# Kernel tuning notes

Hardware: AMD Instinct MI355X
Metric: run time of the kernel (lower is better)

Reference implementation:

```python
import jax, jax.numpy as jnp
import numpy as np

B, P, D = 64, 196, 2048      # batch, num_pixels, encoder_dim
E, H, A = 512, 512, 512      # embed, hidden, attention dims
V, S = 32000, 22             # vocab, caption seq_len


def setup_inputs() -> dict:
    key = jax.random.key(0)
    ks = jax.random.split(key, 24)
    sc = 0.02
    features = jax.random.normal(ks[0], (B, P, D), jnp.float32)
    captions = jax.random.randint(ks[1], (S, B), 0, V)
    caption_lengths = jax.random.randint(ks[2], (B,), 3, S + 1)
    caption_lengths = caption_lengths.at[0].set(S)  # make max static = S
    p = lambda i, shp: sc * jax.random.normal(ks[i], shp, jnp.float32)
    return {
        "features": features,
        "captions": captions,
        "caption_lengths": caption_lengths,
        "emb_W": p(3, (V, E)),
        "We": p(4, (D, A)), "be": p(5, (A,)),
        "Wd": p(6, (H, A)), "bd": p(7, (A,)),
        "wf": p(8, (A, 1)), "bf": p(9, (1,)),
        "Wih": p(10, (4 * H, E + D)), "Whh": p(11, (4 * H, H)),
        "bih": p(12, (4 * H,)), "bhh": p(13, (4 * H,)),
        "Wh0": p(14, (D, H)), "bh0": p(15, (H,)),
        "Wc0": p(16, (D, H)), "bc0": p(17, (H,)),
        "Wbeta": p(18, (H, D)), "bbeta": p(19, (D,)),
        "Wout": p(20, (H, V)), "bout": p(21, (V,)),
    }


def reference(features, captions, caption_lengths, emb_W, We, be, Wd, bd, wf, bf,
              Wih, Whh, bih, bhh, Wh0, bh0, Wc0, bc0, Wbeta, bbeta, Wout, bout):
    # sort batch by caption length, descending
    sort_ind = jnp.argsort(-caption_lengths)
    lens = caption_lengths[sort_ind]
    enc = features[sort_ind]                     # [B,P,D]
    caps = captions.T[sort_ind]                  # [B,S]
    emb = emb_W[caps]                            # [B,S,E]
    mean_enc = enc.mean(axis=1)
    h0 = mean_enc @ Wh0 + bh0
    c0 = mean_enc @ Wc0 + bc0
    decode_lengths = lens - 1
    T = captions.shape[0] - 2                    # max(decode_lengths) - 1, static
    att1 = enc @ We + be                         # [B,P,A], step-invariant
    emb_t = jnp.moveaxis(emb[:, :T, :], 1, 0)    # [T,B,E]
    t_idx = jnp.arange(T)

    def step(carry, inp):
        h, c = carry
        e_t, t = inp
        att2 = h @ Wd + bd                                   # [B,A]
        scores = (jax.nn.relu(att1 + att2[:, None, :]) @ wf)[..., 0] + bf[0]  # [B,P]
        alpha = jax.nn.softmax(scores, axis=1)
        awe = jnp.einsum('bpd,bp->bd', enc, alpha)           # [B,D]
        gate = jax.nn.sigmoid(h @ Wbeta + bbeta)             # [B,D]
        x = jnp.concatenate([e_t, gate * awe], axis=1)       # [B,E+D]
        g = x @ Wih.T + bih + h @ Whh.T + bhh                # [B,4H]
        i, f, gg, o = jnp.split(g, 4, axis=1)                # torch LSTMCell gate order
        c_new = jax.nn.sigmoid(f) * c + jax.nn.sigmoid(i) * jnp.tanh(gg)
        h_new = jax.nn.sigmoid(o) * jnp.tanh(c_new)
        preds = h_new @ Wout + bout                          # [B,V] (dropout in eval = identity)
        m = (decode_lengths > t)[:, None].astype(preds.dtype)
        return (h_new, c_new), (preds * m, alpha * m)

    (_, _), (preds, alphas) = jax.lax.scan(step, (h0, c0), (emb_t, t_idx))
    predictions = jnp.moveaxis(preds, 0, 1)   # [B,T,V]
    alphas = jnp.moveaxis(alphas, 0, 1)       # [B,T,P]
    return predictions, caps, lens, alphas, sort_ind
```

## Files before the change

### kernel.cpp

```cpp
#include <hip/hip_runtime.h>
#include <stdint.h>

typedef short s16x8 __attribute__((ext_vector_type(8)));
typedef short s16x4 __attribute__((ext_vector_type(4)));
typedef float f32x4 __attribute__((ext_vector_type(4)));
typedef unsigned short u16;
typedef unsigned int u32;

#define DEV __device__ __forceinline__

DEV float bf2f(u16 v){ union{float f; unsigned u;} x; x.u = ((unsigned)v)<<16; return x.f; }
DEV u16 f2bf(float f){ union{float f; unsigned u;} x; x.f = f; unsigned r = x.u + 0x7fffu + ((x.u>>16)&1u); return (u16)(r>>16); }
DEV float sigm(float x){ return 1.f/(1.f + __expf(-x)); }

DEV u32  aL(const u32* p){ return __hip_atomic_load(p, __ATOMIC_RELAXED, __HIP_MEMORY_SCOPE_AGENT); }
DEV void aS(u32* p, u32 v){ __hip_atomic_store(p, v, __ATOMIC_RELAXED, __HIP_MEMORY_SCOPE_AGENT); }
DEV float aLf(const float* p){ return __hip_atomic_load(p, __ATOMIC_RELAXED, __HIP_MEMORY_SCOPE_AGENT); }
DEV void aSf(float* p, float v){ __hip_atomic_store(p, v, __ATOMIC_RELAXED, __HIP_MEMORY_SCOPE_AGENT); }


enum { EPI_F32=0, EPI_BF16=1, EPI_H0C0=2, EPI_PREDS=3 };

struct EpiParams {
  float* out0; long ldo;
  u16* outb;
  const float* bias0;
  const int* declen;
  float* c; u16* xh;
};

template<int BM, int BN, int EPI, bool SWAPXY, int SWZM>
__global__ __launch_bounds__(256) void gemm_bt(
    const u16* __restrict__ A, long lda,
    const u16* __restrict__ B, long ldb,
    int K, EpiParams ep)
{
  constexpr int MF = BM/64;
  constexpr int NF = BN/16;
  constexpr int CHA = BM*8, CH = CHA + BN*8;
  constexpr int NST = CH/256;
  __shared__ char smem[(BM+BN)*128];
  const int tid = threadIdx.x;
  const int w = tid>>6, lane = tid&63;

  long arow0, brow0;
  if constexpr (SWZM > 0) {
    int id = blockIdx.x, tot = gridDim.x;
    int q = tot>>3, r = tot&7, xcd = id&7, idx = id>>3;
    int cid = (xcd<r) ? xcd*(q+1)+idx : r*(q+1)+(xcd-r)*q+idx;
    arow0 = (long)(cid % SWZM)*BM; brow0 = (long)(cid / SWZM)*BN;
  } else if constexpr (SWAPXY) { arow0 = (long)blockIdx.x*BM; brow0 = (long)blockIdx.y*BN; }
  else { arow0 = (long)blockIdx.y*BM; brow0 = (long)blockIdx.x*BN; }

  const u16* gsrc[NST]; int ldst[NST];
  #pragma unroll
  for (int i=0;i<NST;++i){
    int c = i*256 + tid;
    if (i*256 < CHA){
      int row = c>>3, k16 = c&7;
      gsrc[i] = A + (arow0+row)*lda + k16*8;
      ldst[i] = row*128 + ((k16*16) ^ ((row&7)<<4));
    } else {
      int cb = c - CHA; int row = cb>>3, k16 = cb&7;
      gsrc[i] = B + (brow0+row)*ldb + k16*8;
      ldst[i] = BM*128 + row*128 + ((k16*16) ^ ((row&7)<<4));
    }
  }

  f32x4 acc[MF][NF];
  #pragma unroll
  for (int i=0;i<MF;++i)
    #pragma unroll
    for (int j=0;j<NF;++j) acc[i][j] = (f32x4){0.f,0.f,0.f,0.f};

  const int KT = K >> 6;
  s16x8 st[NST];
  #pragma unroll
  for (int i=0;i<NST;++i) st[i] = *(const s16x8*)(gsrc[i]);

  char* Al = smem;
  for (int kk=0; kk<KT; ++kk){
    #pragma unroll
    for (int i=0;i<NST;++i) *(s16x8*)(smem + ldst[i]) = st[i];
    __syncthreads();
    if (kk+1 < KT){
      long kb = (long)(kk+1)*64;
      #pragma unroll
      for (int i=0;i<NST;++i) st[i] = *(const s16x8*)(gsrc[i] + kb);
    }
    #pragma unroll
    for (int ks = 0; ks < 2; ++ks) {
      s16x8 af[MF], bfr[NF];
      const int kboff = ks*64 + ((lane>>4)<<4);
      #pragma unroll
      for (int mf=0; mf<MF; ++mf) {
        int r = w*(16*MF) + mf*16 + (lane&15);
        af[mf] = *(const s16x8*)(Al + r*128 + (kboff ^ ((r&7)<<4)));
      }
      #pragma unroll
      for (int nf=0; nf<NF; ++nf) {
        int r = nf*16 + (lane&15);
        bfr[nf] = *(const s16x8*)(Al + BM*128 + r*128 + (kboff ^ ((r&7)<<4)));
      }
      #pragma unroll
      for (int mf=0; mf<MF; ++mf)
        #pragma unroll
        for (int nf=0; nf<NF; ++nf)
          acc[mf][nf] = __builtin_amdgcn_mfma_f32_16x16x32_bf16(bfr[nf], af[mf], acc[mf][nf], 0,0,0);
    }
    __syncthreads();
  }

  #pragma unroll
  for (int mf=0; mf<MF; ++mf)
    #pragma unroll
    for (int nf=0; nf<NF; ++nf){
      long m = arow0 + w*(16*MF) + mf*16 + (lane&15);
      long n0 = brow0 + nf*16 + ((lane>>4)<<2);
      f32x4 bv = *(const f32x4*)&ep.bias0[n0];
      f32x4 v = acc[mf][nf] + bv;
      if constexpr (EPI == EPI_F32) {
        *(f32x4*)&ep.out0[m*ep.ldo + n0] = v;
      } else if constexpr (EPI == EPI_BF16) {
        u16 o[4];
        #pragma unroll
        for (int r=0;r<4;++r) o[r] = f2bf(v[r]);
        *(s16x4*)&ep.outb[m*ep.ldo + n0] = *(s16x4*)o;
      } else if constexpr (EPI == EPI_H0C0) {
        if (n0 < 512){
          u16 o[4];
          #pragma unroll
          for (int r=0;r<4;++r) o[r] = f2bf(v[r]);
          *(s16x4*)&ep.xh[m*2560 + 2048 + n0] = *(s16x4*)o;
        } else {
          *(f32x4*)&ep.c[m*512 + (n0-512)] = v;
        }
      } else {
        int tt = (int)(m>>6), b = (int)(m&63);
        if (ep.declen[b] > tt)
          *(f32x4*)&ep.out0[(long)b*640000 + (long)tt*32000 + n0] = v;
      }
    }
}

DEV void gsync(u32* flags, u32* epochw, u32 ep, int blk, int tid){
  __syncthreads();
  if (blk == 0){
    if (tid == 0) aS(flags, ep);
    if (tid < 256){
      while (aL(flags + tid*16) < ep) __builtin_amdgcn_s_sleep(4);
    }
    __syncthreads();
    if (tid == 0) aS(epochw, ep);
  } else {
    if (tid == 0){
      aS(flags + blk*16, ep);
      while (aL(epochw) < ep) __builtin_amdgcn_s_sleep(8);
    }
    __syncthreads();
  }
}

struct FusedArgs {
  const u16* att1; const u16* enc;
  const u16* wmisc; const u16* wcat2;
  const float* gst; const float* wf; const float* bfp;
  const int* declen; const float* bmisc; const int* nact;
  u16* xh20; float* y0p;
  float* part; int* cnt; float* c; u16* hall;
  float* alph; u32* bar;
};

__global__ __launch_bounds__(512) void steps_fused(FusedArgs fa)
{
  __shared__ char smem[61440];
  __shared__ float wred[8];
  __shared__ int lastf;
  const int blk = blockIdx.x, tid = threadIdx.x;
  const int w = tid>>6, lane = tid&63;
  const int mstrip = w>>1, nhalf = w&1;
  u32* flags = fa.bar;
  u32* epochw = fa.bar + 4096;
  u32 ep = 0;

  for (int t=0; t<20; ++t){
    u16* cur = fa.xh20 + (long)t*163840;
    u16* nxt = cur + 163840;
    u32* cur32 = (u32*)cur;
    u32* nxt32 = (u32*)nxt;

    if (blk < 80){
      const int brow0 = blk*32;
      f32x4 acc = {0,0,0,0};
      #pragma unroll
      for (int r=0; r<2; ++r){
        u32 sa[16];
        #pragma unroll
        for (int i=0;i<16;++i){
          int c = i*512 + tid;
          int row = c>>7, kp = c&127;
          sa[i] = *(const u32*)(cur32 + (long)row*1280 + 1024 + r*128 + kp);
        }
        s16x8 sb[2];
        #pragma unroll
        for (int i=0;i<2;++i){
          int c = i*512 + tid;
          int row = c>>5, k16 = c&31;
          sb[i] = *(const s16x8*)(fa.wmisc + (long)(brow0+row)*512 + r*256 + k16*8);
        }
        #pragma unroll
        for (int i=0;i<16;++i){
          int c = i*512 + tid;
          int row = c>>7, kp = c&127;
          *(u32*)(smem + row*512 + ((kp*4) ^ ((row&7)<<4))) = sa[i];
        }
        #pragma unroll
        for (int i=0;i<2;++i){
          int c = i*512 + tid;
          int row = c>>5, k16 = c&31;
          *(s16x8*)(smem + 32768 + row*512 + ((k16*16) ^ ((row&7)<<4))) = sb[i];
        }
        __syncthreads();
        #pragma unroll
        for (int ks=0; ks<8; ++ks){
          int kboff = ks*64 + ((lane>>4)<<4);
          int ra = mstrip*16 + (lane&15);
          s16x8 af = *(const s16x8*)(smem + ra*512 + (kboff ^ ((ra&7)<<4)));
          int rb = nhalf*16 + (lane&15);
          s16x8 bf = *(const s16x8*)(smem + 32768 + rb*512 + (kboff ^ ((rb&7)<<4)));
          acc = __builtin_amdgcn_mfma_f32_16x16x32_bf16(bf, af, acc, 0,0,0);
        }
        __syncthreads();
      }
      int m = mstrip*16 + (lane&15);
      int n0 = brow0 + nhalf*16 + ((lane>>4)<<2);
      #pragma unroll
      for (int j=0;j<4;++j)
        aSf(fa.y0p + (long)m*2560 + n0 + j, acc[j] + fa.bmisc[n0+j]);
    }
    gsync(flags, epochw, ++ep, blk, tid);

    {
      const int b = blk & 63, s = blk >> 6;
      const int na = fa.nact[t];
      if (b >= na){
        if (s == 0){
          for (int i=tid; i<196; i+=512)
            fa.alph[((long)b*20 + t)*196 + i] = 0.f;
        }
      } else {
      float* att2p = (float*)smem;
      float* wfp   = att2p + 576;
      float* alps  = wfp + 576;
      float* awe_p = alps + 208;
      {
        int kg0 = tid>>6, j = tid&63;
        att2p[kg0*72 + j] = aLf(fa.y0p + (long)b*2560 + 2048 + tid);
        wfp[kg0*72 + j]   = fa.wf[tid];
      }
      __syncthreads();
      const float bfv = fa.bfp[0];
      const int pg = lane>>3, kg = lane&7;
      #pragma unroll
      for (int pass=0; pass<4; ++pass){
        int p = pass*64 + w*8 + pg;
        if (p < 196){
          const u16* ap = fa.att1 + (((long)(b*196 + p))<<9) + kg*64;
          float sa = 0.f;
          #pragma unroll
          for (int i=0;i<8;++i){
            s16x8 v = *(const s16x8*)(ap + i*8);
            #pragma unroll
            for (int q=0;q<8;++q){
              float x = bf2f((u16)v[q]) + att2p[kg*72 + i*8 + q];
              x = fmaxf(x, 0.f);
              sa += x * wfp[kg*72 + i*8 + q];
            }
          }
          sa += __shfl_xor(sa, 1);
          sa += __shfl_xor(sa, 2);
          sa += __shfl_xor(sa, 4);
          if (kg == 0) alps[p] = sa + bfv;
        }
      }
      __syncthreads();
      float v = (tid < 196) ? alps[tid] : -3.4e38f;
      float m8 = v;
      #pragma unroll
      for (int off=32; off; off>>=1) m8 = fmaxf(m8, __shfl_xor(m8, off));
      if (lane == 0) wred[w] = m8;
      __syncthreads();
      float mx = wred[0];
      #pragma unroll
      for (int i=1;i<8;++i) mx = fmaxf(mx, wred[i]);
      float e = (tid < 196) ? __expf(v - mx) : 0.f;
      float s8 = e;
      #pragma unroll
      for (int off=32; off; off>>=1) s8 += __shfl_xor(s8, off);
      __syncthreads();
      if (lane == 0) wred[w] = s8;
      __syncthreads();
      float den = wred[0]+wred[1]+wred[2]+wred[3]+wred[4]+wred[5]+wred[6]+wred[7];
      float inv = 1.f/den;
      if (tid < 196){
        float a = e*inv;
        alps[tid] = a;
        if (s==0) fa.alph[((long)b*20 + t)*196 + tid] = (fa.declen[b] > t) ? a : 0.f;
      }
      __syncthreads();
      const int d0 = s*512 + lane*8;
      const u16* ebase = fa.enc + (((long)b*196)<<11) + d0;
      float a8[8] = {0,0,0,0,0,0,0,0};
      int p = w;
      for (; p+24 < 196; p += 32){
        s16x8 e0 = __builtin_nontemporal_load((const s16x8*)(ebase + ((long)p<<11)));
        s16x8 e1 = __builtin_nontemporal_load((const s16x8*)(ebase + ((long)(p+8)<<11)));
        s16x8 e2 = __builtin_nontemporal_load((const s16x8*)(ebase + ((long)(p+16)<<11)));
        s16x8 e3 = __builtin_nontemporal_load((const s16x8*)(ebase + ((long)(p+24)<<11)));
        float a0 = alps[p], a1 = alps[p+8], a2 = alps[p+16], a3 = alps[p+24];
        #pragma unroll
        for (int q=0;q<8;++q) a8[q] += a0*bf2f((u16)e0[q]);
        #pragma unroll
        for (int q=0;q<8;++q) a8[q] += a1*bf2f((u16)e1[q]);
        #pragma unroll
        for (int q=0;q<8;++q) a8[q] += a2*bf2f((u16)e2[q]);
        #pragma unroll
        for (int q=0;q<8;++q) a8[q] += a3*bf2f((u16)e3[q]);
      }
      for (; p < 196; p += 8){
        s16x8 ev = __builtin_nontemporal_load((const s16x8*)(ebase + ((long)p<<11)));
        float a = alps[p];
        #pragma unroll
        for (int q=0;q<8;++q) a8[q] += a*bf2f((u16)ev[q]);
      }
      *(f32x4*)&awe_p[w*512 + lane*8]     = (f32x4){a8[0],a8[1],a8[2],a8[3]};
      *(f32x4*)&awe_p[w*512 + lane*8 + 4] = (f32x4){a8[4],a8[5],a8[6],a8[7]};
      __syncthreads();
      if (tid < 256){
        int c0 = 2*tid;
        float s0 = 0.f, s1 = 0.f;
        #pragma unroll
        for (int g=0; g<8; ++g){ s0 += awe_p[g*512 + c0]; s1 += awe_p[g*512 + c0 + 1]; }
        float g0 = sigm(aLf(fa.y0p + (long)b*2560 + s*512 + c0));
        float g1 = sigm(aLf(fa.y0p + (long)b*2560 + s*512 + c0 + 1));
        u32 pk = (u32)f2bf(g0*s0) | ((u32)f2bf(g1*s1) << 16);
        aS(cur32 + (long)b*1280 + s*256 + tid, pk);
      }
      __syncthreads();
      }
    }
    gsync(flags, epochw, ++ep, blk, tid);

    {
      const int ntile = blk & 63, split = blk >> 6;
      f32x4 acc = {0,0,0,0};
      #pragma unroll
      for (int r=0; r<2; ++r){
        const int kbw = split*640 + r*320;
        const int kbd = split*320 + r*160;
        u32 sa[20];
        #pragma unroll
        for (int i=0;i<20;++i){
          int c = i*512 + tid;
          int row = c/160, kp = c%160;
          sa[i] = *(const u32*)(cur32 + (long)row*1280 + kbd + kp);
        }
        s16x8 sb[3];
        #pragma unroll
        for (int i=0;i<3;++i){
          int c = i*512 + tid;
          if (c < 1280){
            int row = c/40, k16 = c%40;
            sb[i] = *(const s16x8*)(fa.wcat2 + (long)(ntile*32+row)*2560 + kbw + k16*8);
          }
        }
        #pragma unroll
        for (int i=0;i<20;++i){
          int c = i*512 + tid;
          int row = c/160, kp = c%160;
          *(u32*)(smem + row*640 + ((kp*4) ^ ((row&7)<<4))) = sa[i];
        }
        #pragma unroll
        for (int i=0;i<3;++i){
          int c = i*512 + tid;
          if (c < 1280){
            int row = c/40, k16 = c%40;
            *(s16x8*)(smem + 40960 + row*640 + ((k16*16) ^ ((row&7)<<4))) = sb[i];
          }
        }
        __syncthreads();
        #pragma unroll
        for (int ks=0; ks<10; ++ks){
          int kboff = ks*64 + ((lane>>4)<<4);
          int ra = mstrip*16 + (lane&15);
          s16x8 af = *(const s16x8*)(smem + ra*640 + (kboff ^ ((ra&7)<<4)));
          int rb = nhalf*16 + (lane&15);
          s16x8 bf = *(const s16x8*)(smem + 40960 + rb*640 + (kboff ^ ((rb&7)<<4)));
          acc = __builtin_amdgcn_mfma_f32_16x16x32_bf16(bf, af, acc, 0,0,0);
        }
        __syncthreads();
      }
      {
        float* PS = fa.part + (long)split*(64*2048);
        int m = mstrip*16 + (lane&15);
        int n0 = ntile*32 + nhalf*16 + ((lane>>4)<<2);
        #pragma unroll
        for (int j=0;j<4;++j) aSf(PS + (long)m*2048 + n0 + j, acc[j]);
      }
      __syncthreads();
      if (tid==0){
        int v = __hip_atomic_fetch_add(fa.cnt + t*64 + ntile, 1,
                                       __ATOMIC_RELAXED, __HIP_MEMORY_SCOPE_AGENT);
        lastf = (v == 3);
      }
      __syncthreads();
      if (lastf && tid < 256){
        int b = tid>>2, jp = tid&3;
        u16 h2[2];
        #pragma unroll
        for (int jj=0; jj<2; ++jj){
          int jl = jp*2 + jj;
          int j = ntile*8 + jl;
          float g4[4];
          #pragma unroll
          for (int gi=0; gi<4; ++gi){
            long n = (long)ntile*32 + jl*4 + gi;
            float sg = fa.gst[((long)t*64 + b)*2048 + n];
            #pragma unroll
            for (int sp=0; sp<4; ++sp)
              sg += aLf(fa.part + (long)sp*(64*2048) + (long)b*2048 + n);
            g4[gi] = sg;
          }
          float cc = aLf(fa.c + b*512 + j);
          float cn = sigm(g4[1])*cc + sigm(g4[0])*tanhf(g4[2]);
          float hn = sigm(g4[3])*tanhf(cn);
          aSf(fa.c + b*512 + j, cn);
          h2[jj] = f2bf(hn);
        }
        u32 pk = (u32)h2[0] | ((u32)h2[1] << 16);
        aS(nxt32 + (long)b*1280 + 1024 + ntile*4 + jp, pk);
        *(u32*)&fa.hall[((long)t*64 + b)*512 + ntile*8 + jp*2] = pk;
      }
    }
    if (t < 19) gsync(flags, epochw, ++ep, blk, tid);
  }
}

__global__ __launch_bounds__(256) void transpose_bf16(
    const float* __restrict__ in, u16* __restrict__ out, int R, int C)
{
  __shared__ float t[64][65];
  const int bx = blockIdx.x*64, by = blockIdx.y*64;
  const int tx = threadIdx.x & 63, ty = threadIdx.x >> 6;
  #pragma unroll
  for (int i=0;i<16;++i){ int r = i*4+ty; t[r][tx] = in[(long)(by+r)*C + bx+tx]; }
  __syncthreads();
  #pragma unroll
  for (int i=0;i<16;++i){ int cc = i*4+ty; out[(long)(bx+cc)*R + by+tx] = f2bf(t[tx][cc]); }
}

__global__ void sort_k(const int* __restrict__ cl, const int* __restrict__ captions,
                       int* __restrict__ sidx, int* __restrict__ declen,
                       float* __restrict__ outCaps, float* __restrict__ outLens,
                       float* __restrict__ outSidx, int* __restrict__ cnt,
                       u32* __restrict__ bar, int* __restrict__ nact)
{
  __shared__ int s_idx[64];
  __shared__ int s_dl[64];
  int i = threadIdx.x;
  int li = cl[i];
  int rank = 0;
  for (int j=0;j<64;++j){ int lj = cl[j]; rank += (lj>li) || (lj==li && j<i); }
  s_idx[rank] = i;
  __syncthreads();
  int src = s_idx[i];
  sidx[i] = src;
  int L = cl[src];
  declen[i] = L - 1;
  s_dl[i] = L - 1;
  outLens[i] = (float)L;
  outSidx[i] = (float)src;
  for (int s=0;s<22;++s) outCaps[i*22+s] = (float)captions[s*64 + src];
  for (int s=0;s<20;++s) cnt[s*64 + i] = 0;
  for (int s=i; s<4160; s+=64) bar[s] = 0u;
  __syncthreads();
  if (i < 20){
    int c = 0;
    for (int j=0;j<64;++j) c += (s_dl[j] > i);
    nact[i] = c;
  }
}

__global__ __launch_bounds__(256) void prep_enc(
    const float* __restrict__ features, const int* __restrict__ sidx,
    u16* __restrict__ enc, u16* __restrict__ meanb)
{
  __shared__ float red[4][256];
  int b = blockIdx.x >> 3, oct = blockIdx.x & 7;
  int lv = threadIdx.x & 63, g = threadIdx.x >> 6;
  int d0 = oct*256 + lv*4;
  const float* src = features + (long)sidx[b]*(196*2048) + d0;
  float acc[4] = {0.f,0.f,0.f,0.f};
  for (int p=g; p<196; p+=4){
    f32x4 v = *(const f32x4*)(src + (long)p*2048);
    u16 o[4];
    #pragma unroll
    for (int q=0;q<4;++q){ acc[q] += v[q]; o[q] = f2bf(v[q]); }
    *(s16x4*)(enc + ((long)b*196 + p)*2048 + d0) = *(s16x4*)o;
  }
  #pragma unroll
  for (int q=0;q<4;++q) red[g][lv*4+q] = acc[q];
  __syncthreads();
  if (threadIdx.x < 64){
    u16 mo[4];
    #pragma unroll
    for (int q=0;q<4;++q){
      float s = red[0][threadIdx.x*4+q] + red[1][threadIdx.x*4+q]
              + red[2][threadIdx.x*4+q] + red[3][threadIdx.x*4+q];
      mo[q] = f2bf(s*(1.f/196.f));
    }
    *(s16x4*)(meanb + b*2048 + oct*256 + threadIdx.x*4) = *(s16x4*)mo;
  }
}

__global__ void emb_gather(const int* __restrict__ captions, const int* __restrict__ sidx,
                           const float* __restrict__ embW, u16* __restrict__ out)
{
  int idx = blockIdx.x*256 + threadIdx.x;
  int row = idx >> 6; int e0 = (idx & 63)*8;
  int t = row >> 6, b = row & 63;
  int tok = captions[t*64 + sidx[b]];
  const float* s = embW + (long)tok*512 + e0;
  f32x4 v0 = *(const f32x4*)s, v1 = *(const f32x4*)(s+4);
  u16 o[8];
  #pragma unroll
  for (int q=0;q<4;++q){ o[q] = f2bf(v0[q]); o[4+q] = f2bf(v1[q]); }
  *(s16x8*)(out + (long)row*512 + e0) = *(s16x8*)o;
}

__global__ void build_wcat2(const float* __restrict__ Wih, const float* __restrict__ Whh,
                            u16* __restrict__ out)
{
  long idx = (long)blockIdx.x*256 + threadIdx.x;
  int r = (int)(idx / 320);
  int kc = (int)(idx % 320) * 8;
  int j = r>>2, g = r&3;
  int orow = g*512 + j;
  const float* s = (kc < 2048) ? (Wih + (long)orow*2560 + 512 + kc)
                               : (Whh + (long)orow*512 + (kc - 2048));
  f32x4 v0 = *(const f32x4*)s, v1 = *(const f32x4*)(s+4);
  u16 o[8];
  #pragma unroll
  for (int q=0;q<4;++q){ o[q] = f2bf(v0[q]); o[4+q] = f2bf(v1[q]); }
  *(s16x8*)(out + (long)r*2560 + kc) = *(s16x8*)o;
}

__global__ void build_wihe(const float* __restrict__ Wih, u16* __restrict__ out)
{
  int idx = blockIdx.x*256 + threadIdx.x;
  int r = idx >> 6; int kc = (idx & 63)*8;
  int j = r>>2, g = r&3;
  const float* s = Wih + (long)(g*512+j)*2560 + kc;
  f32x4 v0 = *(const f32x4*)s, v1 = *(const f32x4*)(s+4);
  u16 o[8];
  #pragma unroll
  for (int q=0;q<4;++q){ o[q] = f2bf(v0[q]); o[4+q] = f2bf(v1[q]); }
  *(s16x8*)(out + (long)r*512 + kc) = *(s16x8*)o;
}

__global__ void build_bias(const float* bih, const float* bhh, const float* bbeta,
                           const float* bd, const float* bh0, const float* bc0,
                           float* bstat, float* bmisc, float* bhc)
{
  int idx = blockIdx.x*256 + threadIdx.x;
  if (idx < 2048){ int j = idx>>2, g = idx&3; bstat[idx] = bih[g*512+j] + bhh[g*512+j]; }
  else if (idx < 4608){ int k = idx-2048; bmisc[k] = (k<2048) ? bbeta[k] : bd[k-2048]; }
  else if (idx < 5632){ int k = idx-4608; bhc[k] = (k<512) ? bh0[k] : bc0[k-512]; }
}

static constexpr long OFF_ENC   = 0;
static constexpr long OFF_ATT1  = 51380224;
static constexpr long OFF_WOUTT = 64225280;
static constexpr long OFF_WET   = 96993280;
static constexpr long OFF_WMISC = 99090432;
static constexpr long OFF_WHC   = 101711872;
static constexpr long OFF_WCAT2 = 105906176;
static constexpr long OFF_WIHE  = 116391936;
static constexpr long OFF_EMBB  = 118489088;
static constexpr long OFF_GST   = 119799808;
static constexpr long OFF_HALL  = 130285568;
static constexpr long OFF_MEANB = 131596288;
static constexpr long OFF_C     = 132513792;
static constexpr long OFF_Y0P   = 132644864;
static constexpr long OFF_BSTAT = 133955584;
static constexpr long OFF_BMISC = 133963776;
static constexpr long OFF_BHC   = 133974016;
static constexpr long OFF_SIDX  = 133978112;
static constexpr long OFF_DECL  = 133978368;
static constexpr long OFF_CNT   = 133978624;
static constexpr long OFF_BAR   = 133983744;
static constexpr long OFF_NACT  = 134000384;
static constexpr long OFF_XH20  = 134017024;
static constexpr long OFF_PART  = OFF_WHC;

extern "C" void kernel_launch(void* const* d_in, const int* in_sizes, int n_in,
                              void* d_out, int out_size, void* d_ws, size_t ws_size,
                              hipStream_t stream)
{
  (void)in_sizes; (void)n_in; (void)out_size; (void)ws_size;
  const float* features = (const float*)d_in[0];
  const int*   captions = (const int*)d_in[1];
  const int*   caplen   = (const int*)d_in[2];
  const float* embW     = (const float*)d_in[3];
  const float* We       = (const float*)d_in[4];
  const float* be       = (const float*)d_in[5];
  const float* Wd       = (const float*)d_in[6];
  const float* bd       = (const float*)d_in[7];
  const float* wf       = (const float*)d_in[8];
  const float* bfp      = (const float*)d_in[9];
  const float* Wih      = (const float*)d_in[10];
  const float* Whh      = (const float*)d_in[11];
  const float* bih      = (const float*)d_in[12];
  const float* bhh      = (const float*)d_in[13];
  const float* Wh0      = (const float*)d_in[14];
  const float* bh0      = (const float*)d_in[15];
  const float* Wc0      = (const float*)d_in[16];
  const float* bc0      = (const float*)d_in[17];
  const float* Wbeta    = (const float*)d_in[18];
  const float* bbeta    = (const float*)d_in[19];
  const float* Wout     = (const float*)d_in[20];
  const float* bout     = (const float*)d_in[21];

  char* ws = (char*)d_ws;
  u16*   enc   = (u16*)(ws + OFF_ENC);
  u16*   att1  = (u16*)(ws + OFF_ATT1);
  u16*   woutt = (u16*)(ws + OFF_WOUTT);
  u16*   wet   = (u16*)(ws + OFF_WET);
  u16*   wmisc = (u16*)(ws + OFF_WMISC);
  u16*   whc   = (u16*)(ws + OFF_WHC);
  u16*   wcat2 = (u16*)(ws + OFF_WCAT2);
  u16*   wihe  = (u16*)(ws + OFF_WIHE);
  u16*   embb  = (u16*)(ws + OFF_EMBB);
  float* gst   = (float*)(ws + OFF_GST);
  u16*   hall  = (u16*)(ws + OFF_HALL);
  u16*   meanb = (u16*)(ws + OFF_MEANB);
  float* cbuf  = (float*)(ws + OFF_C);
  float* y0p   = (float*)(ws + OFF_Y0P);
  float* bstat = (float*)(ws + OFF_BSTAT);
  float* bmisc = (float*)(ws + OFF_BMISC);
  float* bhc   = (float*)(ws + OFF_BHC);
  int*   sidx  = (int*)(ws + OFF_SIDX);
  int*   declen= (int*)(ws + OFF_DECL);
  int*   cnt   = (int*)(ws + OFF_CNT);
  u32*   bar   = (u32*)(ws + OFF_BAR);
  int*   nact  = (int*)(ws + OFF_NACT);
  u16*   xh20  = (u16*)(ws + OFF_XH20);
  float* part  = (float*)(ws + OFF_PART);

  float* outP    = (float*)d_out;
  float* outCaps = outP + 40960000;
  float* outLens = outCaps + 1408;
  float* outAlph = outLens + 64;
  float* outSidx = outAlph + 250880;

  sort_k<<<1,64,0,stream>>>(caplen, captions, sidx, declen, outCaps, outLens, outSidx, cnt, bar, nact);
  prep_enc<<<512,256,0,stream>>>(features, sidx, enc, meanb);
  emb_gather<<<320,256,0,stream>>>(captions, sidx, embW, embb);
  transpose_bf16<<<dim3(8,32),256,0,stream>>>(We,    wet,              2048, 512);
  transpose_bf16<<<dim3(32,8),256,0,stream>>>(Wbeta, wmisc,            512, 2048);
  transpose_bf16<<<dim3(8,8), 256,0,stream>>>(Wd,    wmisc + 2048*512, 512, 512);
  transpose_bf16<<<dim3(8,32),256,0,stream>>>(Wh0,   whc,              2048, 512);
  transpose_bf16<<<dim3(8,32),256,0,stream>>>(Wc0,   whc + 512*2048,   2048, 512);
  transpose_bf16<<<dim3(500,8),256,0,stream>>>(Wout, woutt,            512, 32000);
  build_wcat2<<<2560,256,0,stream>>>(Wih, Whh, wcat2);
  build_wihe<<<512,256,0,stream>>>(Wih, wihe);
  build_bias<<<22,256,0,stream>>>(bih,bhh,bbeta,bd,bh0,bc0,bstat,bmisc,bhc);

  { EpiParams ep{}; ep.bias0 = bhc; ep.xh = xh20; ep.c = cbuf;
    gemm_bt<64,64,EPI_H0C0,false,0><<<dim3(16,1),256,0,stream>>>(meanb, 2048, whc, 2048, 2048, ep); }
  { EpiParams ep{}; ep.outb = att1; ep.ldo = 512; ep.bias0 = be;
    gemm_bt<128,128,EPI_BF16,true,0><<<dim3(98,4),256,0,stream>>>(enc, 2048, wet, 2048, 2048, ep); }
  { EpiParams ep{}; ep.out0 = gst; ep.ldo = 2048; ep.bias0 = bstat;
    gemm_bt<128,64,EPI_F32,false,0><<<dim3(32,10),256,0,stream>>>(embb, 512, wihe, 512, 512, ep); }

  {
    FusedArgs fa;
    fa.att1 = att1; fa.enc = enc; fa.wmisc = wmisc; fa.wcat2 = wcat2;
    fa.gst = gst; fa.wf = wf; fa.bfp = bfp; fa.declen = declen; fa.bmisc = bmisc;
    fa.nact = nact;
    fa.xh20 = xh20; fa.y0p = y0p;
    fa.part = part; fa.cnt = cnt; fa.c = cbuf; fa.hall = hall;
    fa.alph = outAlph; fa.bar = bar;
    void* kargs[1] = { &fa };
    hipLaunchCooperativeKernel((const void*)steps_fused, dim3(256), dim3(512),
                               kargs, 0, stream);
  }

  { EpiParams ep{}; ep.out0 = outP; ep.bias0 = bout; ep.declen = declen;
    gemm_bt<128,128,EPI_PREDS,false,10><<<2500,256,0,stream>>>(hall, 512, woutt, 512, 512, ep); }
}
```

Measured before the change: 1.320 ms.

## Fold att2 and gate projections into attention phase, removing a grid barrier per step

Drops the per-step MFMA phase in which 80 blocks computed h@[Wbeta|Wd] into a global buffer, and the grid-wide sync that followed it. Each attention block now computes its own att2 vector and its 512-wide gate slice with a scalar dot product over h, reading a new k-pair-interleaved bf16 weight layout. The partial-sum and cell-state buffers are transposed to a column-major [n][batch] layout for coalesced access, and the alpha masking by decode length is dropped. The cost is redundant weight reads: every block re-reads the Wd column set, and the four blocks of each batch row share the Wbeta slices.

```diff
diff --git a/kernel.cpp b/kernel.cpp
--- a/kernel.cpp
+++ b/kernel.cpp
@@ -133,7 +133,8 @@
           for (int r=0;r<4;++r) o[r] = f2bf(v[r]);
           *(s16x4*)&ep.xh[m*2560 + 2048 + n0] = *(s16x4*)o;
         } else {
-          *(f32x4*)&ep.c[m*512 + (n0-512)] = v;
+          #pragma unroll
+          for (int r=0;r<4;++r) ep.c[(long)(n0-512+r)*64 + m] = v[r];
         }
       } else {
         int tt = (int)(m>>6), b = (int)(m&63);
@@ -163,10 +164,10 @@
 
 struct FusedArgs {
   const u16* att1; const u16* enc;
-  const u16* wmisc; const u16* wcat2;
+  const u32* wmt; const u16* wcat2;
   const float* gst; const float* wf; const float* bfp;
   const int* declen; const float* bmisc; const int* nact;
-  u16* xh20; float* y0p;
+  u16* xh20;
   float* part; int* cnt; float* c; u16* hall;
   float* alph; u32* bar;
 };
@@ -189,57 +190,6 @@
     u32* cur32 = (u32*)cur;
     u32* nxt32 = (u32*)nxt;
 
-    if (blk < 80){
-      const int brow0 = blk*32;
-      f32x4 acc = {0,0,0,0};
-      #pragma unroll
-      for (int r=0; r<2; ++r){
-        u32 sa[16];
-        #pragma unroll
-        for (int i=0;i<16;++i){
-          int c = i*512 + tid;
-          int row = c>>7, kp = c&127;
-          sa[i] = *(const u32*)(cur32 + (long)row*1280 + 1024 + r*128 + kp);
-        }
-        s16x8 sb[2];
-        #pragma unroll
-        for (int i=0;i<2;++i){
-          int c = i*512 + tid;
-          int row = c>>5, k16 = c&31;
-          sb[i] = *(const s16x8*)(fa.wmisc + (long)(brow0+row)*512 + r*256 + k16*8);
-        }
-        #pragma unroll
-        for (int i=0;i<16;++i){
-          int c = i*512 + tid;
-          int row = c>>7, kp = c&127;
-          *(u32*)(smem + row*512 + ((kp*4) ^ ((row&7)<<4))) = sa[i];
-        }
-        #pragma unroll
-        for (int i=0;i<2;++i){
-          int c = i*512 + tid;
-          int row = c>>5, k16 = c&31;
-          *(s16x8*)(smem + 32768 + row*512 + ((k16*16) ^ ((row&7)<<4))) = sb[i];
-        }
-        __syncthreads();
-        #pragma unroll
-        for (int ks=0; ks<8; ++ks){
-          int kboff = ks*64 + ((lane>>4)<<4);
-          int ra = mstrip*16 + (lane&15);
-          s16x8 af = *(const s16x8*)(smem + ra*512 + (kboff ^ ((ra&7)<<4)));
-          int rb = nhalf*16 + (lane&15);
-          s16x8 bf = *(const s16x8*)(smem + 32768 + rb*512 + (kboff ^ ((rb&7)<<4)));
-          acc = __builtin_amdgcn_mfma_f32_16x16x32_bf16(bf, af, acc, 0,0,0);
-        }
-        __syncthreads();
-      }
-      int m = mstrip*16 + (lane&15);
-      int n0 = brow0 + nhalf*16 + ((lane>>4)<<2);
-      #pragma unroll
-      for (int j=0;j<4;++j)
-        aSf(fa.y0p + (long)m*2560 + n0 + j, acc[j] + fa.bmisc[n0+j]);
-    }
-    gsync(flags, epochw, ++ep, blk, tid);
-
     {
       const int b = blk & 63, s = blk >> 6;
       const int na = fa.nact[t];
@@ -253,17 +203,36 @@
       float* wfp   = att2p + 576;
       float* alps  = wfp + 576;
       float* awe_p = alps + 208;
+      float* hs    = awe_p + 4096;
+      float* garr  = hs + 512;
+      if (tid < 256){
+        u32 hp = *(const u32*)(cur32 + (long)b*1280 + 1024 + tid);
+        hs[2*tid]   = bf2f((u16)(hp & 0xffffu));
+        hs[2*tid+1] = bf2f((u16)(hp >> 16));
+      }
+      { int kg0 = tid>>6, j2 = tid&63; wfp[kg0*72 + j2] = fa.wf[tid]; }
+      __syncthreads();
       {
-        int kg0 = tid>>6, j = tid&63;
-        att2p[kg0*72 + j] = aLf(fa.y0p + (long)b*2560 + 2048 + tid);
-        wfp[kg0*72 + j]   = fa.wf[tid];
+        float aacc = 0.f, gacc = 0.f;
+        const u32* wa = fa.wmt + 2048 + tid;
+        const u32* wg = fa.wmt + s*512 + tid;
+        #pragma unroll 4
+        for (int kp = 0; kp < 256; ++kp){
+          u32 pa = wa[(long)kp*2560];
+          u32 pg = wg[(long)kp*2560];
+          float h0 = hs[2*kp], h1 = hs[2*kp+1];
+          aacc += h0*bf2f((u16)(pa&0xffffu)) + h1*bf2f((u16)(pa>>16));
+          gacc += h0*bf2f((u16)(pg&0xffffu)) + h1*bf2f((u16)(pg>>16));
+        }
+        att2p[(tid>>6)*72 + (tid&63)] = aacc + fa.bmisc[2048 + tid];
+        garr[tid] = sigm(gacc + fa.bmisc[s*512 + tid]);
       }
       __syncthreads();
       const float bfv = fa.bfp[0];
-      const int pg = lane>>3, kg = lane&7;
+      const int pg2 = lane>>3, kg = lane&7;
       #pragma unroll
       for (int pass=0; pass<4; ++pass){
-        int p = pass*64 + w*8 + pg;
+        int p = pass*64 + w*8 + pg2;
         if (p < 196){
           const u16* ap = fa.att1 + (((long)(b*196 + p))<<9) + kg*64;
           float sa = 0.f;
@@ -305,7 +274,7 @@
       if (tid < 196){
         float a = e*inv;
         alps[tid] = a;
-        if (s==0) fa.alph[((long)b*20 + t)*196 + tid] = (fa.declen[b] > t) ? a : 0.f;
+        if (s==0) fa.alph[((long)b*20 + t)*196 + tid] = a;
       }
       __syncthreads();
       const int d0 = s*512 + lane*8;
@@ -341,9 +310,7 @@
         float s0 = 0.f, s1 = 0.f;
         #pragma unroll
         for (int g=0; g<8; ++g){ s0 += awe_p[g*512 + c0]; s1 += awe_p[g*512 + c0 + 1]; }
-        float g0 = sigm(aLf(fa.y0p + (long)b*2560 + s*512 + c0));
-        float g1 = sigm(aLf(fa.y0p + (long)b*2560 + s*512 + c0 + 1));
-        u32 pk = (u32)f2bf(g0*s0) | ((u32)f2bf(g1*s1) << 16);
+        u32 pk = (u32)f2bf(garr[c0]*s0) | ((u32)f2bf(garr[c0+1]*s1) << 16);
         aS(cur32 + (long)b*1280 + s*256 + tid, pk);
       }
       __syncthreads();
@@ -401,11 +368,11 @@
         __syncthreads();
       }
       {
-        float* PS = fa.part + (long)split*(64*2048);
+        float* PS = fa.part + (long)split*131072;
         int m = mstrip*16 + (lane&15);
-        int n0 = ntile*32 + nhalf*16 + ((lane>>4)<<2);
-        #pragma unroll
-        for (int j=0;j<4;++j) aSf(PS + (long)m*2048 + n0 + j, acc[j]);
+        int nl = ntile*32 + nhalf*16 + ((lane>>4)<<2);
+        #pragma unroll
+        for (int j=0;j<4;++j) aSf(PS + (long)(nl + j)*64 + m, acc[j]);
       }
       __syncthreads();
       if (tid==0){
@@ -415,31 +382,31 @@
       }
       __syncthreads();
       if (lastf && tid < 256){
-        int b = tid>>2, jp = tid&3;
+        int b2 = tid & 63, jpair = tid >> 6;
         u16 h2[2];
         #pragma unroll
         for (int jj=0; jj<2; ++jj){
-          int jl = jp*2 + jj;
+          int jl = jpair*2 + jj;
           int j = ntile*8 + jl;
           float g4[4];
           #pragma unroll
           for (int gi=0; gi<4; ++gi){
-            long n = (long)ntile*32 + jl*4 + gi;
-            float sg = fa.gst[((long)t*64 + b)*2048 + n];
+            int nl = ntile*32 + jl*4 + gi;
+            float sg = fa.gst[((long)t*64 + b2)*2048 + nl];
             #pragma unroll
             for (int sp=0; sp<4; ++sp)
-              sg += aLf(fa.part + (long)sp*(64*2048) + (long)b*2048 + n);
+              sg += aLf(fa.part + (long)sp*131072 + (long)nl*64 + b2);
             g4[gi] = sg;
           }
-          float cc = aLf(fa.c + b*512 + j);
+          float cc = aLf(fa.c + (long)j*64 + b2);
           float cn = sigm(g4[1])*cc + sigm(g4[0])*tanhf(g4[2]);
           float hn = sigm(g4[3])*tanhf(cn);
-          aSf(fa.c + b*512 + j, cn);
+          aSf(fa.c + (long)j*64 + b2, cn);
           h2[jj] = f2bf(hn);
         }
         u32 pk = (u32)h2[0] | ((u32)h2[1] << 16);
-        aS(nxt32 + (long)b*1280 + 1024 + ntile*4 + jp, pk);
-        *(u32*)&fa.hall[((long)t*64 + b)*512 + ntile*8 + jp*2] = pk;
+        aS(nxt32 + (long)b2*1280 + 1024 + ntile*4 + jpair, pk);
+        *(u32*)&fa.hall[((long)t*64 + b2)*512 + ntile*8 + jpair*2] = pk;
       }
     }
     if (t < 19) gsync(flags, epochw, ++ep, blk, tid);
@@ -555,6 +522,22 @@
   *(s16x8*)(out + (long)r*2560 + kc) = *(s16x8*)o;
 }
 
+__global__ void build_wmt(const float* __restrict__ Wbeta, const float* __restrict__ Wd,
+                          u32* __restrict__ out)
+{
+  long idx = (long)blockIdx.x*256 + threadIdx.x;
+  int kp = (int)(idx / 2560), n = (int)(idx % 2560);
+  float v0, v1;
+  if (n < 2048){
+    v0 = Wbeta[(long)(2*kp)*2048 + n];
+    v1 = Wbeta[(long)(2*kp+1)*2048 + n];
+  } else {
+    v0 = Wd[(long)(2*kp)*512 + (n-2048)];
+    v1 = Wd[(long)(2*kp+1)*512 + (n-2048)];
+  }
+  out[idx] = (u32)f2bf(v0) | ((u32)f2bf(v1) << 16);
+}
+
 __global__ void build_wihe(const float* __restrict__ Wih, u16* __restrict__ out)
 {
   int idx = blockIdx.x*256 + threadIdx.x;
@@ -582,7 +565,7 @@
 static constexpr long OFF_ATT1  = 51380224;
 static constexpr long OFF_WOUTT = 64225280;
 static constexpr long OFF_WET   = 96993280;
-static constexpr long OFF_WMISC = 99090432;
+static constexpr long OFF_WMT   = 99090432;
 static constexpr long OFF_WHC   = 101711872;
 static constexpr long OFF_WCAT2 = 105906176;
 static constexpr long OFF_WIHE  = 116391936;
@@ -591,7 +574,6 @@
 static constexpr long OFF_HALL  = 130285568;
 static constexpr long OFF_MEANB = 131596288;
 static constexpr long OFF_C     = 132513792;
-static constexpr long OFF_Y0P   = 132644864;
 static constexpr long OFF_BSTAT = 133955584;
 static constexpr long OFF_BMISC = 133963776;
 static constexpr long OFF_BHC   = 133974016;
@@ -636,7 +618,7 @@
   u16*   att1  = (u16*)(ws + OFF_ATT1);
   u16*   woutt = (u16*)(ws + OFF_WOUTT);
   u16*   wet   = (u16*)(ws + OFF_WET);
-  u16*   wmisc = (u16*)(ws + OFF_WMISC);
+  u32*   wmt   = (u32*)(ws + OFF_WMT);
   u16*   whc   = (u16*)(ws + OFF_WHC);
   u16*   wcat2 = (u16*)(ws + OFF_WCAT2);
   u16*   wihe  = (u16*)(ws + OFF_WIHE);
@@ -645,7 +627,6 @@
   u16*   hall  = (u16*)(ws + OFF_HALL);
   u16*   meanb = (u16*)(ws + OFF_MEANB);
   float* cbuf  = (float*)(ws + OFF_C);
-  float* y0p   = (float*)(ws + OFF_Y0P);
   float* bstat = (float*)(ws + OFF_BSTAT);
   float* bmisc = (float*)(ws + OFF_BMISC);
   float* bhc   = (float*)(ws + OFF_BHC);
@@ -666,13 +647,12 @@
   sort_k<<<1,64,0,stream>>>(caplen, captions, sidx, declen, outCaps, outLens, outSidx, cnt, bar, nact);
   prep_enc<<<512,256,0,stream>>>(features, sidx, enc, meanb);
   emb_gather<<<320,256,0,stream>>>(captions, sidx, embW, embb);
-  transpose_bf16<<<dim3(8,32),256,0,stream>>>(We,    wet,              2048, 512);
-  transpose_bf16<<<dim3(32,8),256,0,stream>>>(Wbeta, wmisc,            512, 2048);
-  transpose_bf16<<<dim3(8,8), 256,0,stream>>>(Wd,    wmisc + 2048*512, 512, 512);
-  transpose_bf16<<<dim3(8,32),256,0,stream>>>(Wh0,   whc,              2048, 512);
-  transpose_bf16<<<dim3(8,32),256,0,stream>>>(Wc0,   whc + 512*2048,   2048, 512);
-  transpose_bf16<<<dim3(500,8),256,0,stream>>>(Wout, woutt,            512, 32000);
+  transpose_bf16<<<dim3(8,32),256,0,stream>>>(We,  wet, 2048, 512);
+  transpose_bf16<<<dim3(8,32),256,0,stream>>>(Wh0, whc, 2048, 512);
+  transpose_bf16<<<dim3(8,32),256,0,stream>>>(Wc0, whc + 512*2048, 2048, 512);
+  transpose_bf16<<<dim3(500,8),256,0,stream>>>(Wout, woutt, 512, 32000);
   build_wcat2<<<2560,256,0,stream>>>(Wih, Whh, wcat2);
+  build_wmt<<<2560,256,0,stream>>>(Wbeta, Wd, wmt);
   build_wihe<<<512,256,0,stream>>>(Wih, wihe);
   build_bias<<<22,256,0,stream>>>(bih,bhh,bbeta,bd,bh0,bc0,bstat,bmisc,bhc);
 
@@ -685,10 +665,10 @@
 
   {
     FusedArgs fa;
-    fa.att1 = att1; fa.enc = enc; fa.wmisc = wmisc; fa.wcat2 = wcat2;
+    fa.att1 = att1; fa.enc = enc; fa.wmt = wmt; fa.wcat2 = wcat2;
     fa.gst = gst; fa.wf = wf; fa.bfp = bfp; fa.declen = declen; fa.bmisc = bmisc;
     fa.nact = nact;
-    fa.xh20 = xh20; fa.y0p = y0p;
+    fa.xh20 = xh20;
     fa.part = part; fa.cnt = cnt; fa.c = cbuf; fa.hall = hall;
     fa.alph = outAlph; fa.bar = bar;
     void* kargs[1] = { &fa };
```

Measured after the change: 2.773 ms. +110.1%, slower.

## Replace global barriers with per-stage dependency counters in fused step kernel

Applied to the files above, without the earlier changes.

Swaps the centralized flag/epoch grid barrier for per-step atomic counters. Each phase now waits only on the counter of the producer stage it depends on: phase 1 waits on h completion from 64 last-finisher blocks, phase 2 waits on 80 phase-1 blocks, and phase 3 waits on 256 blocks. This removes the two-hop barrier through block 0 and lets blocks that have no work in a phase run ahead. The risk is memory-ordering problems, because only relaxed atomics are used with no fences, and it relies on the bar buffer being zeroed and having enough slots for the counters.

```diff
diff --git a/kernel.cpp b/kernel.cpp
--- a/kernel.cpp
+++ b/kernel.cpp
@@ -143,22 +143,16 @@
     }
 }
 
-DEV void gsync(u32* flags, u32* epochw, u32 ep, int blk, int tid){
+DEV void wait_cnt(const u32* p, u32 tgt){
+  if (threadIdx.x == 0){
+    while (aL(p) < tgt) __builtin_amdgcn_s_sleep(4);
+  }
   __syncthreads();
-  if (blk == 0){
-    if (tid == 0) aS(flags, ep);
-    if (tid < 256){
-      while (aL(flags + tid*16) < ep) __builtin_amdgcn_s_sleep(4);
-    }
-    __syncthreads();
-    if (tid == 0) aS(epochw, ep);
-  } else {
-    if (tid == 0){
-      aS(flags + blk*16, ep);
-      while (aL(epochw) < ep) __builtin_amdgcn_s_sleep(8);
-    }
-    __syncthreads();
-  }
+}
+DEV void bump(u32* p){
+  __syncthreads();
+  if (threadIdx.x == 0)
+    __hip_atomic_fetch_add(p, 1u, __ATOMIC_RELAXED, __HIP_MEMORY_SCOPE_AGENT);
 }
 
 struct FusedArgs {
@@ -179,9 +173,9 @@
   const int blk = blockIdx.x, tid = threadIdx.x;
   const int w = tid>>6, lane = tid&63;
   const int mstrip = w>>1, nhalf = w&1;
-  u32* flags = fa.bar;
-  u32* epochw = fa.bar + 4096;
-  u32 ep = 0;
+  u32* p1c = fa.bar;
+  u32* xc  = fa.bar + 64;
+  u32* hc  = fa.bar + 128;
 
   for (int t=0; t<20; ++t){
     u16* cur = fa.xh20 + (long)t*163840;
@@ -190,6 +184,7 @@
     u32* nxt32 = (u32*)nxt;
 
     if (blk < 80){
+      if (t > 0) wait_cnt(hc + (t-1), 64);
       const int brow0 = blk*32;
       f32x4 acc = {0,0,0,0};
       #pragma unroll
@@ -237,9 +232,10 @@
       #pragma unroll
       for (int j=0;j<4;++j)
         aSf(fa.y0p + (long)m*2560 + n0 + j, acc[j] + fa.bmisc[n0+j]);
-    }
-    gsync(flags, epochw, ++ep, blk, tid);
-
+      bump(p1c + t);
+    }
+
+    wait_cnt(p1c + t, 80);
     {
       const int b = blk & 63, s = blk >> 6;
       const int na = fa.nact[t];
@@ -346,11 +342,11 @@
         u32 pk = (u32)f2bf(g0*s0) | ((u32)f2bf(g1*s1) << 16);
         aS(cur32 + (long)b*1280 + s*256 + tid, pk);
       }
-      __syncthreads();
-      }
-    }
-    gsync(flags, epochw, ++ep, blk, tid);
-
+      }
+    }
+    bump(xc + t);
+
+    wait_cnt(xc + t, 256);
     {
       const int ntile = blk & 63, split = blk >> 6;
       f32x4 acc = {0,0,0,0};
@@ -441,8 +437,10 @@
         aS(nxt32 + (long)b*1280 + 1024 + ntile*4 + jp, pk);
         *(u32*)&fa.hall[((long)t*64 + b)*512 + ntile*8 + jp*2] = pk;
       }
-    }
-    if (t < 19) gsync(flags, epochw, ++ep, blk, tid);
+      __syncthreads();
+      if (lastf && tid == 0)
+        __hip_atomic_fetch_add(hc + t, 1u, __ATOMIC_RELAXED, __HIP_MEMORY_SCOPE_AGENT);
+    }
   }
 }
 
```

New measurement: 1.534 ms. +16.2%, slower.
